# Kernel optimization log

Hardware: AMD Instinct MI355X
Metric: run time of the kernel (lower is better)

Reference implementation:

```python
import jax, jax.numpy as jnp
import numpy as np

P = 128

def setup_inputs() -> dict:
    key = jax.random.key(0)
    k1, k2 = jax.random.split(key)
    N = 2_000_128
    y_serie = jax.random.normal(k1, (N,), dtype=jnp.float32)
    params = jax.random.normal(k2, (P,), dtype=jnp.float32)
    return {"y_serie": y_serie, "params": params}

def reference(y_serie, params):
    p = params.shape[0]
    n = y_serie.shape[0] - p  # number of prediction rows
    # Toeplitz lag matrix Y[i, j] = y[i + j], built with one vectorized gather
    idx = jnp.arange(n)[:, None] + jnp.arange(p)[None, :]  # (n, p)
    Y = y_serie[idx]                                       # (n, p)
    pred = Y @ params                                      # (n,)
    loss = jnp.mean((pred - y_serie[p:]) ** 2) + jnp.sum(jnp.abs(params))
    return (pred, loss)
```

## Files before the change

kernel.cpp:

```cpp
#include <hip/hip_runtime.h>

#define P 128
#define BLOCK 256
#define RPT 4
#define TILE (BLOCK * RPT)
#define STAGE (TILE + P)

__global__ __launch_bounds__(BLOCK) void ar_pred_kernel(
    const float* __restrict__ y, const float* __restrict__ params,
    float* __restrict__ out, float* __restrict__ partials,
    int n, int Ntot)
{
    __shared__ float ylds[STAGE];
    __shared__ float plds[P];
    __shared__ float red[BLOCK / 64];

    const int t = threadIdx.x;
    const int tile0 = blockIdx.x * TILE;

    if (t < P) plds[t] = params[t];

    if (tile0 + STAGE <= Ntot) {
        const float4* src = (const float4*)(y + tile0);
        float4* dst = (float4*)ylds;
        dst[t] = src[t];
        if (t < STAGE / 4 - BLOCK) dst[t + BLOCK] = src[t + BLOCK];
    } else {
        for (int idx = t; idx < STAGE; idx += BLOCK) {
            int g = tile0 + idx;
            ylds[idx] = (g < Ntot) ? y[g] : 0.f;
        }
    }
    __syncthreads();

    const int l0 = t * RPT;
    float4 w0 = *(const float4*)&ylds[l0];
    float a0 = 0.f, a1 = 0.f, a2 = 0.f, a3 = 0.f;
    #pragma unroll
    for (int j = 0; j < P; j += 4) {
        float4 w1 = *(const float4*)&ylds[l0 + j + 4];
        float4 pj = *(const float4*)&plds[j];
        a0 = fmaf(w0.x, pj.x, a0); a1 = fmaf(w0.y, pj.x, a1);
        a2 = fmaf(w0.z, pj.x, a2); a3 = fmaf(w0.w, pj.x, a3);
        a0 = fmaf(w0.y, pj.y, a0); a1 = fmaf(w0.z, pj.y, a1);
        a2 = fmaf(w0.w, pj.y, a2); a3 = fmaf(w1.x, pj.y, a3);
        a0 = fmaf(w0.z, pj.z, a0); a1 = fmaf(w0.w, pj.z, a1);
        a2 = fmaf(w1.x, pj.z, a2); a3 = fmaf(w1.y, pj.z, a3);
        a0 = fmaf(w0.w, pj.w, a0); a1 = fmaf(w1.x, pj.w, a1);
        a2 = fmaf(w1.y, pj.w, a2); a3 = fmaf(w1.z, pj.w, a3);
        w0 = w1;
    }

    const int i0 = tile0 + l0;
    float sq = 0.f;
    if (i0 < n) {
        float r0 = a0 - ylds[l0 + 0 + P];
        float r1 = a1 - ylds[l0 + 1 + P];
        float r2 = a2 - ylds[l0 + 2 + P];
        float r3 = a3 - ylds[l0 + 3 + P];
        sq = r0 * r0 + r1 * r1 + r2 * r2 + r3 * r3;
        float4 o; o.x = a0; o.y = a1; o.z = a2; o.w = a3;
        *(float4*)(out + i0) = o;
    }

    #pragma unroll
    for (int off = 32; off >= 1; off >>= 1)
        sq += __shfl_down(sq, off, 64);
    if ((t & 63) == 0) red[t >> 6] = sq;
    __syncthreads();
    if (t == 0)
        partials[blockIdx.x] = red[0] + red[1] + red[2] + red[3];
}

__global__ __launch_bounds__(256) void ar_finalize(
    const float* __restrict__ params, const float* __restrict__ partials,
    float* __restrict__ out, int n, int nblocks)
{
    __shared__ float redsq[4];
    __shared__ float redl1[4];
    const int t = threadIdx.x;

    float sq = 0.f;
    for (int i = t; i < nblocks; i += 256) sq += partials[i];
    float l1 = (t < P) ? fabsf(params[t]) : 0.f;

    #pragma unroll
    for (int off = 32; off >= 1; off >>= 1) {
        sq += __shfl_down(sq, off, 64);
        l1 += __shfl_down(l1, off, 64);
    }
    if ((t & 63) == 0) { redsq[t >> 6] = sq; redl1[t >> 6] = l1; }
    __syncthreads();
    if (t == 0) {
        float s = redsq[0] + redsq[1] + redsq[2] + redsq[3];
        float a = redl1[0] + redl1[1] + redl1[2] + redl1[3];
        out[n] = s / (float)n + a;
    }
}

extern "C" void kernel_launch(void* const* d_in, const int* in_sizes, int n_in,
                              void* d_out, int out_size, void* d_ws, size_t ws_size,
                              hipStream_t stream)
{
    const float* y      = (const float*)d_in[0];
    const float* params = (const float*)d_in[1];
    float* out      = (float*)d_out;
    float* partials = (float*)d_ws;

    const int Ntot = in_sizes[0];
    const int n    = Ntot - P;

    const int nblocks = (n + TILE - 1) / TILE;
    ar_pred_kernel<<<nblocks, BLOCK, 0, stream>>>(y, params, out, partials, n, Ntot);
    ar_finalize<<<1, 256, 0, stream>>>(params, partials, out, n, nblocks);
}
```

Baseline: 85.19 us.

## Compute eight outputs per thread with swizzled LDS and scalar param loads

```diff
diff --git a/kernel.cpp b/kernel.cpp
--- a/kernel.cpp
+++ b/kernel.cpp
@@ -2,65 +2,81 @@
 
 #define P 128
 #define BLOCK 256
-#define RPT 4
+#define RPT 8
 #define TILE (BLOCK * RPT)
 #define STAGE (TILE + P)
+#define NSLOT (STAGE / 4)
+
+__device__ __forceinline__ int swz(int u) { return u ^ ((u >> 3) & 1); }
 
 __global__ __launch_bounds__(BLOCK) void ar_pred_kernel(
     const float* __restrict__ y, const float* __restrict__ params,
     float* __restrict__ out, float* __restrict__ partials,
     int n, int Ntot)
 {
-    __shared__ float ylds[STAGE];
-    __shared__ float plds[P];
+    __shared__ float4 ylds[NSLOT];
     __shared__ float red[BLOCK / 64];
 
     const int t = threadIdx.x;
     const int tile0 = blockIdx.x * TILE;
 
-    if (t < P) plds[t] = params[t];
-
     if (tile0 + STAGE <= Ntot) {
         const float4* src = (const float4*)(y + tile0);
-        float4* dst = (float4*)ylds;
-        dst[t] = src[t];
-        if (t < STAGE / 4 - BLOCK) dst[t + BLOCK] = src[t + BLOCK];
+        ylds[swz(t)]       = src[t];
+        ylds[swz(t + 256)] = src[t + 256];
+        if (t < NSLOT - 512) ylds[swz(t + 512)] = src[t + 512];
     } else {
+        float* yl = (float*)ylds;
         for (int idx = t; idx < STAGE; idx += BLOCK) {
             int g = tile0 + idx;
-            ylds[idx] = (g < Ntot) ? y[g] : 0.f;
+            yl[idx ^ (((idx >> 5) & 1) << 2)] = (g < Ntot) ? y[g] : 0.f;
         }
     }
     __syncthreads();
 
-    const int l0 = t * RPT;
-    float4 w0 = *(const float4*)&ylds[l0];
-    float a0 = 0.f, a1 = 0.f, a2 = 0.f, a3 = 0.f;
+    const int base  = t * RPT;
+    const int ubase = base >> 2;
+
+    float wv[12];
+    {
+        float4 a = ylds[swz(ubase)];
+        float4 b = ylds[swz(ubase + 1)];
+        wv[0] = a.x; wv[1] = a.y; wv[2] = a.z; wv[3] = a.w;
+        wv[4] = b.x; wv[5] = b.y; wv[6] = b.z; wv[7] = b.w;
+    }
+    float acc[RPT];
     #pragma unroll
-    for (int j = 0; j < P; j += 4) {
-        float4 w1 = *(const float4*)&ylds[l0 + j + 4];
-        float4 pj = *(const float4*)&plds[j];
-        a0 = fmaf(w0.x, pj.x, a0); a1 = fmaf(w0.y, pj.x, a1);
-        a2 = fmaf(w0.z, pj.x, a2); a3 = fmaf(w0.w, pj.x, a3);
-        a0 = fmaf(w0.y, pj.y, a0); a1 = fmaf(w0.z, pj.y, a1);
-        a2 = fmaf(w0.w, pj.y, a2); a3 = fmaf(w1.x, pj.y, a3);
-        a0 = fmaf(w0.z, pj.z, a0); a1 = fmaf(w0.w, pj.z, a1);
-        a2 = fmaf(w1.x, pj.z, a2); a3 = fmaf(w1.y, pj.z, a3);
-        a0 = fmaf(w0.w, pj.w, a0); a1 = fmaf(w1.x, pj.w, a1);
-        a2 = fmaf(w1.y, pj.w, a2); a3 = fmaf(w1.z, pj.w, a3);
-        w0 = w1;
+    for (int m = 0; m < RPT; ++m) acc[m] = 0.f;
+
+    #pragma unroll
+    for (int jj = 0; jj < P / 4; ++jj) {
+        float4 c = ylds[swz(ubase + 2 + jj)];
+        wv[8] = c.x; wv[9] = c.y; wv[10] = c.z; wv[11] = c.w;
+        #pragma unroll
+        for (int k = 0; k < 4; ++k) {
+            const float p = params[jj * 4 + k];
+            #pragma unroll
+            for (int m = 0; m < RPT; ++m)
+                acc[m] = fmaf(wv[k + m], p, acc[m]);
+        }
+        #pragma unroll
+        for (int i = 0; i < 8; ++i) wv[i] = wv[i + 4];
     }
 
-    const int i0 = tile0 + l0;
+    const int i0 = tile0 + base;
     float sq = 0.f;
     if (i0 < n) {
-        float r0 = a0 - ylds[l0 + 0 + P];
-        float r1 = a1 - ylds[l0 + 1 + P];
-        float r2 = a2 - ylds[l0 + 2 + P];
-        float r3 = a3 - ylds[l0 + 3 + P];
-        sq = r0 * r0 + r1 * r1 + r2 * r2 + r3 * r3;
-        float4 o; o.x = a0; o.y = a1; o.z = a2; o.w = a3;
-        *(float4*)(out + i0) = o;
+        float4 t0 = ylds[swz(ubase + 32)];
+        float4 t1 = ylds[swz(ubase + 33)];
+        float r0 = acc[0] - t0.x, r1 = acc[1] - t0.y;
+        float r2 = acc[2] - t0.z, r3 = acc[3] - t0.w;
+        float r4 = acc[4] - t1.x, r5 = acc[5] - t1.y;
+        float r6 = acc[6] - t1.z, r7 = acc[7] - t1.w;
+        sq = r0*r0 + r1*r1 + r2*r2 + r3*r3 + r4*r4 + r5*r5 + r6*r6 + r7*r7;
+        float4 o0; o0.x = acc[0]; o0.y = acc[1]; o0.z = acc[2]; o0.w = acc[3];
+        float4 o1; o1.x = acc[4]; o1.y = acc[5]; o1.z = acc[6]; o1.w = acc[7];
+        *(float4*)(out + i0)     = o0;
+        *(float4*)(out + i0 + 4) = o1;
     }
 
     #pragma unroll
```

After: 69.45 us. 1.23x faster.
